# Optimization experiments

Measured on AMD Instinct MI355X. Metric: run time of the kernel, lower is better.

The kernel has to match this reference:

```python
import jax, jax.numpy as jnp
import numpy as np

N_NODES = 100000


def _add_self_loops(edge_index, n):
    loop = jnp.arange(n, dtype=edge_index.dtype)
    src = jnp.concatenate([edge_index[0], loop])
    dst = jnp.concatenate([edge_index[1], loop])
    return src, dst


def _gcn_conv(x, src, dst, n, W, b):
    # PyG GCNConv: linear first, then sym-normalized aggregation, then bias.
    h = x @ W                                   # [N, out]
    deg = jnp.zeros((n,), h.dtype).at[dst].add(1.0)   # in-degree incl. self-loops
    dinv = jnp.where(deg > 0, jax.lax.rsqrt(deg), 0.0)
    norm = dinv[src] * dinv[dst]                # [E+N]
    msg = h[src] * norm[:, None]                # gather + scale
    out = jax.ops.segment_sum(msg, dst, num_segments=n)  # scatter-add
    return out + b


def setup_inputs() -> dict:
    key = jax.random.key(0)
    ks = jax.random.split(key, 9)
    n, d_in, d_h, d_out = N_NODES, 64, 64, 64
    x = jax.random.normal(ks[0], (n, d_in), jnp.float32)
    edge_index = jax.random.randint(ks[1], (2, 1200000), 0, n, jnp.int64)
    s = lambda k, sh: jax.random.normal(k, sh, jnp.float32) * (1.0 / np.sqrt(sh[0]))
    return {
        "x": x,
        "edge_index": edge_index,
        "W1": s(ks[2], (d_in, d_h)),
        "b1": jnp.zeros((d_h,), jnp.float32),
        "W2": s(ks[3], (d_h, d_out)),
        "b2": jnp.zeros((d_out,), jnp.float32),
        "Wl": s(ks[4], (d_out, d_out)),
        "bl": jnp.zeros((d_out,), jnp.float32),
    }


def reference(x, edge_index, W1, b1, W2, b2, Wl, bl):
    n = x.shape[0]
    src, dst = _add_self_loops(edge_index, n)
    h = _gcn_conv(x, src, dst, n, W1, b1)
    h = jax.nn.relu(h)
    h = _gcn_conv(h, src, dst, n, W2, b2)
    return h @ Wl + bl
```

## Files before the change

kernel.cpp:

```cpp
#include <hip/hip_runtime.h>
#include <hip/hip_bf16.h>


#define FEAT 64

typedef __attribute__((ext_vector_type(8))) short bf16x8;
typedef __attribute__((ext_vector_type(4))) float f32x4;
union BF8 { bf16x8 v; unsigned short u[8]; unsigned pk[4]; uint4 q; };

__device__ __forceinline__ unsigned short f2bf(float f) {
    unsigned u = __float_as_uint(f);
    return (unsigned short)((u + 0x7FFFu + ((u >> 16) & 1u)) >> 16);
}
__device__ __forceinline__ float bflo(unsigned u) { return __uint_as_float(u << 16); }
__device__ __forceinline__ float bfhi(unsigned u) { return __uint_as_float(u & 0xFFFF0000u); }
__device__ __forceinline__ unsigned pk2bf(float a, float b) {
    union { __hip_bfloat162 b; unsigned u; } cv;
    cv.b = __float22bfloat162_rn(make_float2(a, b));
    return cv.u;
}

__global__ void k_prepw(const float* __restrict__ W1, const float* __restrict__ W2,
                        const float* __restrict__ Wl, unsigned short* __restrict__ P,
                        int* __restrict__ bcnt) {
    if (blockIdx.x == 3) {
        if (threadIdx.x < 256) bcnt[threadIdx.x] = 0;
        return;
    }
    const float* W = (blockIdx.x == 0) ? W1 : (blockIdx.x == 1) ? W2 : Wl;
    unsigned short* p = P + blockIdx.x * 4096;
    for (int i = threadIdx.x; i < 4096; i += 256) {
        int c = i >> 10, s = (i >> 9) & 1, l = (i >> 3) & 63, j = i & 7;
        int k = s * 32 + ((l >> 4) << 3) + j;
        int col = ((l & 15) << 2) + c;
        p[i] = f2bf(W[k * 64 + col]);
    }
}

__global__ void __launch_bounds__(256)
k_bhist(const int* __restrict__ dst, int* __restrict__ bcnt, int E) {
    __shared__ int h[256];
    int tid = threadIdx.x;
    h[tid] = 0;
    __syncthreads();
    int stride = gridDim.x * 256;
    for (int e = blockIdx.x * 256 + tid; e < E; e += stride)
        atomicAdd(&h[dst[e] >> 9], 1);
    __syncthreads();
    if (h[tid]) atomicAdd(&bcnt[tid], h[tid]);
}

__global__ void k_bscan(const int* __restrict__ bcnt, int* __restrict__ bbase,
                        int* __restrict__ bcur) {
    __shared__ int s[256];
    int t = threadIdx.x;
    int v = bcnt[t];
    s[t] = v;
    __syncthreads();
    for (int off = 1; off < 256; off <<= 1) {
        int x = (t >= off) ? s[t - off] : 0;
        __syncthreads();
        s[t] += x;
        __syncthreads();
    }
    int ex = s[t] - v;
    bbase[t] = ex;
    bcur[t] = ex;
    if (t == 255) bbase[256] = s[255];
}

__global__ void __launch_bounds__(256)
k_part(const int* __restrict__ src, const int* __restrict__ dst,
       int* __restrict__ bcur, unsigned* __restrict__ pass1, int E) {
    __shared__ unsigned pk[4096];
    __shared__ unsigned char bk[4096];
    __shared__ int h[256];
    __shared__ int cur[256];
    int tid = threadIdx.x;
    h[tid] = 0;
    __syncthreads();
    int base = blockIdx.x * 4096;
#pragma unroll
    for (int i = 0; i < 16; ++i) {
        int li = i * 256 + tid;
        int e = base + li;
        if (e < E) {
            int s = src[e], d = dst[e];
            int b = d >> 9;
            pk[li] = ((unsigned)s << 9) | ((unsigned)d & 511u);
            bk[li] = (unsigned char)b;
            atomicAdd(&h[b], 1);
        } else {
            bk[li] = 255;
            pk[li] = 0xFFFFFFFFu;
        }
    }
    __syncthreads();
    {
        int c = h[tid];
        int run = c ? atomicAdd(&bcur[tid], c) : 0;
        cur[tid] = run;
    }
    __syncthreads();
#pragma unroll
    for (int i = 0; i < 16; ++i) {
        int li = i * 256 + tid;
        int e = base + li;
        if (e < E) {
            int b = bk[li];
            int pos = atomicAdd(&cur[b], 1);
            pass1[pos] = pk[li];
        }
    }
}

__global__ void __launch_bounds__(512)
k_csr(const unsigned* __restrict__ pass1, const int* __restrict__ bbase,
      int* __restrict__ offs, float* __restrict__ dinv, int* __restrict__ esrc,
      int n, int E) {
    __shared__ int hist[512];
    __shared__ int cur[512];
    int tid = threadIdx.x;
    int b = blockIdx.x;
    hist[tid] = 0;
    __syncthreads();
    int beg = bbase[b], end = bbase[b + 1];
    for (int j = beg + tid; j < end; j += 512)
        atomicAdd(&hist[pass1[j] & 511u], 1);
    __syncthreads();
    int v = hist[tid];
    for (int off = 1; off < 512; off <<= 1) {
        int x = (tid >= off) ? hist[tid - off] : 0;
        __syncthreads();
        hist[tid] += x;
        __syncthreads();
    }
    int excl = hist[tid] - v;
    int node = (b << 9) + tid;
    if (node < n) {
        offs[node] = beg + excl;
        dinv[node] = rsqrtf((float)v + 1.0f);
    }
    cur[tid] = excl;
    if (b == 0 && tid == 0) offs[n] = E;
    __syncthreads();
    for (int j = beg + tid; j < end; j += 512) {
        unsigned u = pass1[j];
        int loc = (int)(u & 511u);
        int r = atomicAdd(&cur[loc], 1);
        esrc[beg + r] = (int)(u >> 9);
    }
}

template <bool IN_BF16, bool OUT_F32, bool SCALE>
__global__ void __launch_bounds__(256)
k_gemm_mfma(const void* __restrict__ Xv, const unsigned short* __restrict__ Wpk,
            const float* __restrict__ bias, const float* __restrict__ rowscale,
            void* __restrict__ Hv, int n) {
    int lane = threadIdx.x & 63;
    int wid = (blockIdx.x << 2) + (threadIdx.x >> 6);
    int nw = gridDim.x << 2;
    int T = (n + 15) >> 4;
    BF8 bfr[8];
    const uint4* wp = (const uint4*)Wpk;
#pragma unroll
    for (int f = 0; f < 8; ++f) bfr[f].q = wp[f * 64 + lane];
    int mrow = lane & 15, kq = lane >> 4, colb = lane & 15;
    float4 bv4 = make_float4(0.f, 0.f, 0.f, 0.f);
    if (OUT_F32) bv4 = ((const float4*)bias)[colb];
    for (int t = wid; t < T; t += nw) {
        int rb = t << 4;
        int row = rb + mrow;
        bool ok = row < n;
        BF8 a0, a1;
        if (IN_BF16) {
            const uint4* xr = (const uint4*)((const unsigned short*)Xv + ((unsigned)row << 6));
            a0.q = ok ? xr[kq]     : make_uint4(0, 0, 0, 0);
            a1.q = ok ? xr[kq + 4] : make_uint4(0, 0, 0, 0);
        } else {
            const float4* xr = (const float4*)((const float*)Xv + ((unsigned)row << 6));
            float4 z = make_float4(0.f, 0.f, 0.f, 0.f);
            float4 p0 = ok ? xr[kq * 2]     : z;
            float4 p1 = ok ? xr[kq * 2 + 1] : z;
            float4 p2 = ok ? xr[8 + kq * 2] : z;
            float4 p3 = ok ? xr[8 + kq * 2 + 1] : z;
            a0.pk[0] = pk2bf(p0.x, p0.y); a0.pk[1] = pk2bf(p0.z, p0.w);
            a0.pk[2] = pk2bf(p1.x, p1.y); a0.pk[3] = pk2bf(p1.z, p1.w);
            a1.pk[0] = pk2bf(p2.x, p2.y); a1.pk[1] = pk2bf(p2.z, p2.w);
            a1.pk[2] = pk2bf(p3.x, p3.y); a1.pk[3] = pk2bf(p3.z, p3.w);
        }
        f32x4 acc0 = {0.f, 0.f, 0.f, 0.f}, acc1 = acc0, acc2 = acc0, acc3 = acc0;
        acc0 = __builtin_amdgcn_mfma_f32_16x16x32_bf16(a0.v, bfr[0].v, acc0, 0, 0, 0);
        acc0 = __builtin_amdgcn_mfma_f32_16x16x32_bf16(a1.v, bfr[1].v, acc0, 0, 0, 0);
        acc1 = __builtin_amdgcn_mfma_f32_16x16x32_bf16(a0.v, bfr[2].v, acc1, 0, 0, 0);
        acc1 = __builtin_amdgcn_mfma_f32_16x16x32_bf16(a1.v, bfr[3].v, acc1, 0, 0, 0);
        acc2 = __builtin_amdgcn_mfma_f32_16x16x32_bf16(a0.v, bfr[4].v, acc2, 0, 0, 0);
        acc2 = __builtin_amdgcn_mfma_f32_16x16x32_bf16(a1.v, bfr[5].v, acc2, 0, 0, 0);
        acc3 = __builtin_amdgcn_mfma_f32_16x16x32_bf16(a0.v, bfr[6].v, acc3, 0, 0, 0);
        acc3 = __builtin_amdgcn_mfma_f32_16x16x32_bf16(a1.v, bfr[7].v, acc3, 0, 0, 0);
        int rowb = rb + (kq << 2);
        if (OUT_F32) {
            float* O = (float*)Hv;
#pragma unroll
            for (int i = 0; i < 4; ++i) {
                if (rowb + i >= n) break;
                unsigned ro = (unsigned)(rowb + i) << 6;
                float4 o = make_float4(acc0[i] + bv4.x, acc1[i] + bv4.y,
                                       acc2[i] + bv4.z, acc3[i] + bv4.w);
                *(float4*)(O + ro + (colb << 2)) = o;
            }
        } else {
            unsigned short* O = (unsigned short*)Hv;
#pragma unroll
            for (int i = 0; i < 4; ++i) {
                if (rowb + i >= n) break;
                float sc = SCALE ? rowscale[rowb + i] : 1.0f;
                unsigned ro = (unsigned)(rowb + i) << 6;
                uint2 o = make_uint2(pk2bf(acc0[i] * sc, acc1[i] * sc),
                                     pk2bf(acc2[i] * sc, acc3[i] * sc));
                *(uint2*)(O + ro + (colb << 2)) = o;
            }
        }
    }
}

template <bool RELU>
__global__ void __launch_bounds__(256)
k_agg(const int* __restrict__ offs, const int* __restrict__ esrc,
      const float* __restrict__ dinv, const unsigned short* __restrict__ Hs,
      const float* __restrict__ bias, unsigned short* __restrict__ out, int n) {
    int lane = threadIdx.x & 63;
    int h8 = lane & 7;
    int node = blockIdx.x * 32 + ((threadIdx.x >> 6) << 3) + (lane >> 3);
    bool nok = node < n;
    int beg = 0, end = 0;
    if (nok) { beg = offs[node]; end = offs[node + 1]; }
    float a0 = 0.f, a1 = 0.f, a2 = 0.f, a3 = 0.f, a4 = 0.f, a5 = 0.f, a6 = 0.f, a7 = 0.f;
    int j = beg;
    int s0 = 0, s1 = 0, s2 = 0, s3 = 0;
    float w0 = 0.f, w1 = 0.f, w2 = 0.f, w3 = 0.f;
    if (j     < end) { s0 = esrc[j];     w0 = 1.f; }
    if (j + 1 < end) { s1 = esrc[j + 1]; w1 = 1.f; }
    if (j + 2 < end) { s2 = esrc[j + 2]; w2 = 1.f; }
    if (j + 3 < end) { s3 = esrc[j + 3]; w3 = 1.f; }
    while (__ballot(j < end)) {
        uint4 h0 = *(const uint4*)(Hs + ((unsigned)s0 << 6) + (h8 << 3));
        uint4 h1 = *(const uint4*)(Hs + ((unsigned)s1 << 6) + (h8 << 3));
        uint4 h2 = *(const uint4*)(Hs + ((unsigned)s2 << 6) + (h8 << 3));
        uint4 h3 = *(const uint4*)(Hs + ((unsigned)s3 << 6) + (h8 << 3));
        int jn = j + 4;
        int t0 = s0, t1 = s1, t2 = s2, t3 = s3;
        float v0 = 0.f, v1 = 0.f, v2 = 0.f, v3 = 0.f;
        if (jn     < end) { t0 = esrc[jn];     v0 = 1.f; }
        if (jn + 1 < end) { t1 = esrc[jn + 1]; v1 = 1.f; }
        if (jn + 2 < end) { t2 = esrc[jn + 2]; v2 = 1.f; }
        if (jn + 3 < end) { t3 = esrc[jn + 3]; v3 = 1.f; }
        a0 = fmaf(bflo(h0.x), w0, a0); a1 = fmaf(bfhi(h0.x), w0, a1);
        a2 = fmaf(bflo(h0.y), w0, a2); a3 = fmaf(bfhi(h0.y), w0, a3);
        a4 = fmaf(bflo(h0.z), w0, a4); a5 = fmaf(bfhi(h0.z), w0, a5);
        a6 = fmaf(bflo(h0.w), w0, a6); a7 = fmaf(bfhi(h0.w), w0, a7);
        a0 = fmaf(bflo(h1.x), w1, a0); a1 = fmaf(bfhi(h1.x), w1, a1);
        a2 = fmaf(bflo(h1.y), w1, a2); a3 = fmaf(bfhi(h1.y), w1, a3);
        a4 = fmaf(bflo(h1.z), w1, a4); a5 = fmaf(bfhi(h1.z), w1, a5);
        a6 = fmaf(bflo(h1.w), w1, a6); a7 = fmaf(bfhi(h1.w), w1, a7);
        a0 = fmaf(bflo(h2.x), w2, a0); a1 = fmaf(bfhi(h2.x), w2, a1);
        a2 = fmaf(bflo(h2.y), w2, a2); a3 = fmaf(bfhi(h2.y), w2, a3);
        a4 = fmaf(bflo(h2.z), w2, a4); a5 = fmaf(bfhi(h2.z), w2, a5);
        a6 = fmaf(bflo(h2.w), w2, a6); a7 = fmaf(bfhi(h2.w), w2, a7);
        a0 = fmaf(bflo(h3.x), w3, a0); a1 = fmaf(bfhi(h3.x), w3, a1);
        a2 = fmaf(bflo(h3.y), w3, a2); a3 = fmaf(bfhi(h3.y), w3, a3);
        a4 = fmaf(bflo(h3.z), w3, a4); a5 = fmaf(bfhi(h3.z), w3, a5);
        a6 = fmaf(bflo(h3.w), w3, a6); a7 = fmaf(bfhi(h3.w), w3, a7);
        j = jn;
        s0 = t0; s1 = t1; s2 = t2; s3 = t3;
        w0 = v0; w1 = v1; w2 = v2; w3 = v3;
    }
    if (nok) {
        float dd = dinv[node];
        uint4 sv = *(const uint4*)(Hs + ((unsigned)node << 6) + (h8 << 3));
        const float4* b4 = (const float4*)bias;
        float4 bA = b4[h8 * 2], bB = b4[h8 * 2 + 1];
        float r0 = (a0 + bflo(sv.x)) * dd + bA.x;
        float r1 = (a1 + bfhi(sv.x)) * dd + bA.y;
        float r2 = (a2 + bflo(sv.y)) * dd + bA.z;
        float r3 = (a3 + bfhi(sv.y)) * dd + bA.w;
        float r4 = (a4 + bflo(sv.z)) * dd + bB.x;
        float r5 = (a5 + bfhi(sv.z)) * dd + bB.y;
        float r6 = (a6 + bflo(sv.w)) * dd + bB.z;
        float r7 = (a7 + bfhi(sv.w)) * dd + bB.w;
        if (RELU) {
            r0 = fmaxf(r0, 0.f); r1 = fmaxf(r1, 0.f); r2 = fmaxf(r2, 0.f); r3 = fmaxf(r3, 0.f);
            r4 = fmaxf(r4, 0.f); r5 = fmaxf(r5, 0.f); r6 = fmaxf(r6, 0.f); r7 = fmaxf(r7, 0.f);
        }
        uint4 o = make_uint4(pk2bf(r0, r1), pk2bf(r2, r3), pk2bf(r4, r5), pk2bf(r6, r7));
        *(uint4*)(out + ((unsigned)node << 6) + (h8 << 3)) = o;
    }
}

extern "C" void kernel_launch(void* const* d_in, const int* in_sizes, int n_in,
                              void* d_out, int out_size, void* d_ws, size_t ws_size,
                              hipStream_t stream) {
    const float* x  = (const float*)d_in[0];
    const int*   ei = (const int*)d_in[1];
    const float* W1 = (const float*)d_in[2];
    const float* b1 = (const float*)d_in[3];
    const float* W2 = (const float*)d_in[4];
    const float* b2 = (const float*)d_in[5];
    const float* Wl = (const float*)d_in[6];
    const float* bl = (const float*)d_in[7];
    float* out = (float*)d_out;

    const int n = in_sizes[0] / FEAT;
    const int E = in_sizes[1] / 2;
    const int* src = ei;
    const int* dst = ei + E;

    const int B = 256;
    const int NB = (n + 511) >> 9;
    const int pblocks = (E + 4095) / 4096;
    const int agg_blocks  = (n + 31) / 32;
    const int T = (n + 15) / 16;
    const int gemm_blocks = (T + 7) / 8;

    char* w = (char*)d_ws;
    int*   bcnt     = (int*)w;              w += 256 * 4;
    int*   bbase    = (int*)w;              w += 260 * 4;
    int*   bcur     = (int*)w;              w += 256 * 4;
    int*   offs     = (int*)w;              w += ((size_t)n + 4) * 4;
    float* dinv     = (float*)w;            w += (size_t)n * 4;
    w = (char*)(((uintptr_t)w + 15) & ~(uintptr_t)15);
    unsigned short* Wpk = (unsigned short*)w;  w += 3 * 4096 * 2;
    unsigned* pass1 = (unsigned*)w;         w += (size_t)E * 4;
    int*   esrc     = (int*)w;              w += (size_t)E * 4;
    unsigned short* bufA = (unsigned short*)w;  w += (size_t)n * FEAT * 2;
    unsigned short* bufB = (unsigned short*)w;

    k_prepw<<<dim3(4), dim3(B), 0, stream>>>(W1, W2, Wl, Wpk, bcnt);

    k_bhist<<<dim3(256), dim3(B), 0, stream>>>(dst, bcnt, E);
    k_bscan<<<dim3(1), dim3(B), 0, stream>>>(bcnt, bbase, bcur);
    k_part<<<dim3(pblocks), dim3(B), 0, stream>>>(src, dst, bcur, pass1, E);
    k_csr<<<dim3(NB), dim3(512), 0, stream>>>(pass1, bbase, offs, dinv, esrc, n, E);

    k_gemm_mfma<false, false, true><<<dim3(gemm_blocks), dim3(B), 0, stream>>>(x, Wpk, nullptr, dinv, bufA, n);
    k_agg<true><<<dim3(agg_blocks), dim3(B), 0, stream>>>(offs, esrc, dinv, bufA, b1, bufB, n);

    k_gemm_mfma<true, false, true><<<dim3(gemm_blocks), dim3(B), 0, stream>>>(bufB, Wpk + 4096, nullptr, dinv, bufA, n);
    k_agg<false><<<dim3(agg_blocks), dim3(B), 0, stream>>>(offs, esrc, dinv, bufA, b2, bufB, n);

    k_gemm_mfma<true, true, false><<<dim3(gemm_blocks), dim3(B), 0, stream>>>(bufB, Wpk + 8192, bl, nullptr, out, n);
}
```

Before: 251.5 us.

## Fuse aggregation with following GEMM and degree-sort nodes for load balance

Aggregation kernels now apply the next layer's weight matrix via MFMA on an LDS tile, removing two standalone GEMM launches and the round trip of intermediate features through memory. Nodes within each 512-node bucket are reordered by in-degree (perm, pofs, pdinv) so that lanes in a wave share similar edge counts and spend less time idle. The weight prep is merged into the partition kernel as extra blocks, and the bucket histogram writes per-block partials instead of using global atomics, which drops the bcnt zeroing launch. The cost is indirect permuted writes, extra per-node metadata, and a block-wide sync inside the aggregation.

```diff
diff --git a/kernel.cpp b/kernel.cpp
--- a/kernel.cpp
+++ b/kernel.cpp
@@ -3,6 +3,7 @@
 
 
 #define FEAT 64
+#define NBH 128
 
 typedef __attribute__((ext_vector_type(8))) short bf16x8;
 typedef __attribute__((ext_vector_type(4))) float f32x4;
@@ -20,25 +21,8 @@
     return cv.u;
 }
 
-__global__ void k_prepw(const float* __restrict__ W1, const float* __restrict__ W2,
-                        const float* __restrict__ Wl, unsigned short* __restrict__ P,
-                        int* __restrict__ bcnt) {
-    if (blockIdx.x == 3) {
-        if (threadIdx.x < 256) bcnt[threadIdx.x] = 0;
-        return;
-    }
-    const float* W = (blockIdx.x == 0) ? W1 : (blockIdx.x == 1) ? W2 : Wl;
-    unsigned short* p = P + blockIdx.x * 4096;
-    for (int i = threadIdx.x; i < 4096; i += 256) {
-        int c = i >> 10, s = (i >> 9) & 1, l = (i >> 3) & 63, j = i & 7;
-        int k = s * 32 + ((l >> 4) << 3) + j;
-        int col = ((l & 15) << 2) + c;
-        p[i] = f2bf(W[k * 64 + col]);
-    }
-}
-
 __global__ void __launch_bounds__(256)
-k_bhist(const int* __restrict__ dst, int* __restrict__ bcnt, int E) {
+k_bhist(const int* __restrict__ dst, int* __restrict__ bh, int E) {
     __shared__ int h[256];
     int tid = threadIdx.x;
     h[tid] = 0;
@@ -47,14 +31,15 @@
     for (int e = blockIdx.x * 256 + tid; e < E; e += stride)
         atomicAdd(&h[dst[e] >> 9], 1);
     __syncthreads();
-    if (h[tid]) atomicAdd(&bcnt[tid], h[tid]);
-}
-
-__global__ void k_bscan(const int* __restrict__ bcnt, int* __restrict__ bbase,
+    bh[blockIdx.x * 256 + tid] = h[tid];
+}
+
+__global__ void k_bscan(const int* __restrict__ bh, int* __restrict__ bbase,
                         int* __restrict__ bcur) {
     __shared__ int s[256];
     int t = threadIdx.x;
-    int v = bcnt[t];
+    int v = 0;
+    for (int b = 0; b < NBH; ++b) v += bh[b * 256 + t];
     s[t] = v;
     __syncthreads();
     for (int off = 1; off < 256; off <<= 1) {
@@ -71,7 +56,21 @@
 
 __global__ void __launch_bounds__(256)
 k_part(const int* __restrict__ src, const int* __restrict__ dst,
-       int* __restrict__ bcur, unsigned* __restrict__ pass1, int E) {
+       int* __restrict__ bcur, unsigned* __restrict__ pass1, int E, int pblocks,
+       const float* __restrict__ W1, const float* __restrict__ W2,
+       const float* __restrict__ Wl, unsigned short* __restrict__ P) {
+    if ((int)blockIdx.x >= pblocks) {
+        int widx = blockIdx.x - pblocks;
+        const float* W = (widx == 0) ? W1 : (widx == 1) ? W2 : Wl;
+        unsigned short* p = P + widx * 4096;
+        for (int i = threadIdx.x; i < 4096; i += 256) {
+            int c = i >> 10, s = (i >> 9) & 1, l = (i >> 3) & 63, j = i & 7;
+            int k = s * 32 + ((l >> 4) << 3) + j;
+            int col = ((l & 15) << 2) + c;
+            p[i] = f2bf(W[k * 64 + col]);
+        }
+        return;
+    }
     __shared__ unsigned pk[4096];
     __shared__ unsigned char bk[4096];
     __shared__ int h[256];
@@ -116,13 +115,18 @@
 
 __global__ void __launch_bounds__(512)
 k_csr(const unsigned* __restrict__ pass1, const int* __restrict__ bbase,
-      int* __restrict__ offs, float* __restrict__ dinv, int* __restrict__ esrc,
+      float* __restrict__ dinv, int* __restrict__ esrc,
+      int* __restrict__ perm, int2* __restrict__ pofs, float* __restrict__ pdinv,
       int n, int E) {
     __shared__ int hist[512];
     __shared__ int cur[512];
+    __shared__ int dh[64];
+    __shared__ int dbase[64];
+    __shared__ int dcur[64];
     int tid = threadIdx.x;
     int b = blockIdx.x;
     hist[tid] = 0;
+    if (tid < 64) dh[tid] = 0;
     __syncthreads();
     int beg = bbase[b], end = bbase[b + 1];
     for (int j = beg + tid; j < end; j += 512)
@@ -137,13 +141,26 @@
     }
     int excl = hist[tid] - v;
     int node = (b << 9) + tid;
-    if (node < n) {
-        offs[node] = beg + excl;
+    bool valid = node < n;
+    if (valid) {
         dinv[node] = rsqrtf((float)v + 1.0f);
+        atomicAdd(&dh[min(v, 63)], 1);
     }
     cur[tid] = excl;
-    if (b == 0 && tid == 0) offs[n] = E;
-    __syncthreads();
+    __syncthreads();
+    if (tid == 0) {
+        int run = 0;
+        for (int i = 0; i < 64; ++i) { dbase[i] = run; run += dh[i]; dcur[i] = 0; }
+    }
+    __syncthreads();
+    if (valid) {
+        int bin = min(v, 63);
+        int r = atomicAdd(&dcur[bin], 1);
+        int gs = (b << 9) + dbase[bin] + r;
+        perm[gs] = node;
+        pofs[gs] = make_int2(beg + excl, beg + excl + v);
+        pdinv[gs] = rsqrtf((float)v + 1.0f);
+    }
     for (int j = beg + tid; j < end; j += 512) {
         unsigned u = pass1[j];
         int loc = (int)(u & 511u);
@@ -224,61 +241,84 @@
     }
 }
 
-template <bool RELU>
+template <bool RELU, bool OUT_F32>
 __global__ void __launch_bounds__(256)
-k_agg(const int* __restrict__ offs, const int* __restrict__ esrc,
-      const float* __restrict__ dinv, const unsigned short* __restrict__ Hs,
-      const float* __restrict__ bias, unsigned short* __restrict__ out, int n) {
-    int lane = threadIdx.x & 63;
+k_fagg(const int* __restrict__ perm, const int2* __restrict__ pofs,
+       const float* __restrict__ pdinv, const int* __restrict__ esrc,
+       const unsigned short* __restrict__ Hs, const float* __restrict__ bias1,
+       const unsigned short* __restrict__ Wpk, const float* __restrict__ bias2,
+       void* __restrict__ outv, int n) {
+    __shared__ uint4 lds_a[32][8];
+    int tid = threadIdx.x;
+    int lane = tid & 63;
+    int wv = tid >> 6;
     int h8 = lane & 7;
-    int node = blockIdx.x * 32 + ((threadIdx.x >> 6) << 3) + (lane >> 3);
-    bool nok = node < n;
-    int beg = 0, end = 0;
-    if (nok) { beg = offs[node]; end = offs[node + 1]; }
+    int rl = (wv << 3) + (lane >> 3);
+    int slot = blockIdx.x * 32 + rl;
+    bool ok = slot < n;
+    int node = 0, beg = 0, end = 0;
+    float dd = 0.f;
+    if (ok) {
+        node = perm[slot];
+        int2 oe = pofs[slot];
+        beg = oe.x; end = oe.y;
+        dd = pdinv[slot];
+    }
+    int hh = wv & 1, tt = wv >> 1;
+    BF8 bq0, bq1, bq2, bq3;
+    {
+        const uint4* wp = (const uint4*)Wpk;
+        bq0.q = wp[(4 * hh + 0) * 64 + lane];
+        bq1.q = wp[(4 * hh + 1) * 64 + lane];
+        bq2.q = wp[(4 * hh + 2) * 64 + lane];
+        bq3.q = wp[(4 * hh + 3) * 64 + lane];
+    }
     float a0 = 0.f, a1 = 0.f, a2 = 0.f, a3 = 0.f, a4 = 0.f, a5 = 0.f, a6 = 0.f, a7 = 0.f;
-    int j = beg;
-    int s0 = 0, s1 = 0, s2 = 0, s3 = 0;
-    float w0 = 0.f, w1 = 0.f, w2 = 0.f, w3 = 0.f;
-    if (j     < end) { s0 = esrc[j];     w0 = 1.f; }
-    if (j + 1 < end) { s1 = esrc[j + 1]; w1 = 1.f; }
-    if (j + 2 < end) { s2 = esrc[j + 2]; w2 = 1.f; }
-    if (j + 3 < end) { s3 = esrc[j + 3]; w3 = 1.f; }
-    while (__ballot(j < end)) {
-        uint4 h0 = *(const uint4*)(Hs + ((unsigned)s0 << 6) + (h8 << 3));
-        uint4 h1 = *(const uint4*)(Hs + ((unsigned)s1 << 6) + (h8 << 3));
-        uint4 h2 = *(const uint4*)(Hs + ((unsigned)s2 << 6) + (h8 << 3));
-        uint4 h3 = *(const uint4*)(Hs + ((unsigned)s3 << 6) + (h8 << 3));
-        int jn = j + 4;
-        int t0 = s0, t1 = s1, t2 = s2, t3 = s3;
-        float v0 = 0.f, v1 = 0.f, v2 = 0.f, v3 = 0.f;
-        if (jn     < end) { t0 = esrc[jn];     v0 = 1.f; }
-        if (jn + 1 < end) { t1 = esrc[jn + 1]; v1 = 1.f; }
-        if (jn + 2 < end) { t2 = esrc[jn + 2]; v2 = 1.f; }
-        if (jn + 3 < end) { t3 = esrc[jn + 3]; v3 = 1.f; }
-        a0 = fmaf(bflo(h0.x), w0, a0); a1 = fmaf(bfhi(h0.x), w0, a1);
-        a2 = fmaf(bflo(h0.y), w0, a2); a3 = fmaf(bfhi(h0.y), w0, a3);
-        a4 = fmaf(bflo(h0.z), w0, a4); a5 = fmaf(bfhi(h0.z), w0, a5);
-        a6 = fmaf(bflo(h0.w), w0, a6); a7 = fmaf(bfhi(h0.w), w0, a7);
-        a0 = fmaf(bflo(h1.x), w1, a0); a1 = fmaf(bfhi(h1.x), w1, a1);
-        a2 = fmaf(bflo(h1.y), w1, a2); a3 = fmaf(bfhi(h1.y), w1, a3);
-        a4 = fmaf(bflo(h1.z), w1, a4); a5 = fmaf(bfhi(h1.z), w1, a5);
-        a6 = fmaf(bflo(h1.w), w1, a6); a7 = fmaf(bfhi(h1.w), w1, a7);
-        a0 = fmaf(bflo(h2.x), w2, a0); a1 = fmaf(bfhi(h2.x), w2, a1);
-        a2 = fmaf(bflo(h2.y), w2, a2); a3 = fmaf(bfhi(h2.y), w2, a3);
-        a4 = fmaf(bflo(h2.z), w2, a4); a5 = fmaf(bfhi(h2.z), w2, a5);
-        a6 = fmaf(bflo(h2.w), w2, a6); a7 = fmaf(bfhi(h2.w), w2, a7);
-        a0 = fmaf(bflo(h3.x), w3, a0); a1 = fmaf(bfhi(h3.x), w3, a1);
-        a2 = fmaf(bflo(h3.y), w3, a2); a3 = fmaf(bfhi(h3.y), w3, a3);
-        a4 = fmaf(bflo(h3.z), w3, a4); a5 = fmaf(bfhi(h3.z), w3, a5);
-        a6 = fmaf(bflo(h3.w), w3, a6); a7 = fmaf(bfhi(h3.w), w3, a7);
-        j = jn;
-        s0 = t0; s1 = t1; s2 = t2; s3 = t3;
-        w0 = v0; w1 = v1; w2 = v2; w3 = v3;
-    }
-    if (nok) {
-        float dd = dinv[node];
+    {
+        int j = beg;
+        int s0 = 0, s1 = 0, s2 = 0, s3 = 0;
+        float w0 = 0.f, w1 = 0.f, w2 = 0.f, w3 = 0.f;
+        if (j     < end) { s0 = esrc[j];     w0 = 1.f; }
+        if (j + 1 < end) { s1 = esrc[j + 1]; w1 = 1.f; }
+        if (j + 2 < end) { s2 = esrc[j + 2]; w2 = 1.f; }
+        if (j + 3 < end) { s3 = esrc[j + 3]; w3 = 1.f; }
+        while (__ballot(j < end)) {
+            uint4 h0 = *(const uint4*)(Hs + ((unsigned)s0 << 6) + (h8 << 3));
+            uint4 h1 = *(const uint4*)(Hs + ((unsigned)s1 << 6) + (h8 << 3));
+            uint4 h2 = *(const uint4*)(Hs + ((unsigned)s2 << 6) + (h8 << 3));
+            uint4 h3 = *(const uint4*)(Hs + ((unsigned)s3 << 6) + (h8 << 3));
+            int jn = j + 4;
+            int t0 = s0, t1 = s1, t2 = s2, t3 = s3;
+            float v0 = 0.f, v1 = 0.f, v2 = 0.f, v3 = 0.f;
+            if (jn     < end) { t0 = esrc[jn];     v0 = 1.f; }
+            if (jn + 1 < end) { t1 = esrc[jn + 1]; v1 = 1.f; }
+            if (jn + 2 < end) { t2 = esrc[jn + 2]; v2 = 1.f; }
+            if (jn + 3 < end) { t3 = esrc[jn + 3]; v3 = 1.f; }
+            a0 = fmaf(bflo(h0.x), w0, a0); a1 = fmaf(bfhi(h0.x), w0, a1);
+            a2 = fmaf(bflo(h0.y), w0, a2); a3 = fmaf(bfhi(h0.y), w0, a3);
+            a4 = fmaf(bflo(h0.z), w0, a4); a5 = fmaf(bfhi(h0.z), w0, a5);
+            a6 = fmaf(bflo(h0.w), w0, a6); a7 = fmaf(bfhi(h0.w), w0, a7);
+            a0 = fmaf(bflo(h1.x), w1, a0); a1 = fmaf(bfhi(h1.x), w1, a1);
+            a2 = fmaf(bflo(h1.y), w1, a2); a3 = fmaf(bfhi(h1.y), w1, a3);
+            a4 = fmaf(bflo(h1.z), w1, a4); a5 = fmaf(bfhi(h1.z), w1, a5);
+            a6 = fmaf(bflo(h1.w), w1, a6); a7 = fmaf(bfhi(h1.w), w1, a7);
+            a0 = fmaf(bflo(h2.x), w2, a0); a1 = fmaf(bfhi(h2.x), w2, a1);
+            a2 = fmaf(bflo(h2.y), w2, a2); a3 = fmaf(bfhi(h2.y), w2, a3);
+            a4 = fmaf(bflo(h2.z), w2, a4); a5 = fmaf(bfhi(h2.z), w2, a5);
+            a6 = fmaf(bflo(h2.w), w2, a6); a7 = fmaf(bfhi(h2.w), w2, a7);
+            a0 = fmaf(bflo(h3.x), w3, a0); a1 = fmaf(bfhi(h3.x), w3, a1);
+            a2 = fmaf(bflo(h3.y), w3, a2); a3 = fmaf(bfhi(h3.y), w3, a3);
+            a4 = fmaf(bflo(h3.z), w3, a4); a5 = fmaf(bfhi(h3.z), w3, a5);
+            a6 = fmaf(bflo(h3.w), w3, a6); a7 = fmaf(bfhi(h3.w), w3, a7);
+            j = jn;
+            s0 = t0; s1 = t1; s2 = t2; s3 = t3;
+            w0 = v0; w1 = v1; w2 = v2; w3 = v3;
+        }
+    }
+    uint4 packed = make_uint4(0, 0, 0, 0);
+    if (ok) {
         uint4 sv = *(const uint4*)(Hs + ((unsigned)node << 6) + (h8 << 3));
-        const float4* b4 = (const float4*)bias;
+        const float4* b4 = (const float4*)bias1;
         float4 bA = b4[h8 * 2], bB = b4[h8 * 2 + 1];
         float r0 = (a0 + bflo(sv.x)) * dd + bA.x;
         float r1 = (a1 + bfhi(sv.x)) * dd + bA.y;
@@ -292,8 +332,39 @@
             r0 = fmaxf(r0, 0.f); r1 = fmaxf(r1, 0.f); r2 = fmaxf(r2, 0.f); r3 = fmaxf(r3, 0.f);
             r4 = fmaxf(r4, 0.f); r5 = fmaxf(r5, 0.f); r6 = fmaxf(r6, 0.f); r7 = fmaxf(r7, 0.f);
         }
-        uint4 o = make_uint4(pk2bf(r0, r1), pk2bf(r2, r3), pk2bf(r4, r5), pk2bf(r6, r7));
-        *(uint4*)(out + ((unsigned)node << 6) + (h8 << 3)) = o;
+        packed = make_uint4(pk2bf(r0, r1), pk2bf(r2, r3), pk2bf(r4, r5), pk2bf(r6, r7));
+    }
+    lds_a[rl][h8 ^ (rl & 7)] = packed;
+    __syncthreads();
+    int mr = lane & 15, kq = lane >> 4, colb = lane & 15;
+    int rloc = tt * 16 + mr;
+    BF8 fa0, fa1;
+    fa0.q = lds_a[rloc][kq ^ (rloc & 7)];
+    fa1.q = lds_a[rloc][(kq + 4) ^ (rloc & 7)];
+    f32x4 accA = {0.f, 0.f, 0.f, 0.f}, accB = accA;
+    accA = __builtin_amdgcn_mfma_f32_16x16x32_bf16(fa0.v, bq0.v, accA, 0, 0, 0);
+    accA = __builtin_amdgcn_mfma_f32_16x16x32_bf16(fa1.v, bq1.v, accA, 0, 0, 0);
+    accB = __builtin_amdgcn_mfma_f32_16x16x32_bf16(fa0.v, bq2.v, accB, 0, 0, 0);
+    accB = __builtin_amdgcn_mfma_f32_16x16x32_bf16(fa1.v, bq3.v, accB, 0, 0, 0);
+    float b2x = 0.f, b2y = 0.f;
+    if (OUT_F32) {
+        b2x = bias2[(colb << 2) + (hh << 1)];
+        b2y = bias2[(colb << 2) + (hh << 1) + 1];
+    }
+    int rowb = tt * 16 + (kq << 2);
+#pragma unroll
+    for (int i = 0; i < 4; ++i) {
+        int sl = blockIdx.x * 32 + rowb + i;
+        if (sl >= n) break;
+        int orow = perm[sl];
+        if (OUT_F32) {
+            float2 o = make_float2(accA[i] + b2x, accB[i] + b2y);
+            *(float2*)((float*)outv + ((unsigned)orow << 6) + (colb << 2) + (hh << 1)) = o;
+        } else {
+            float sc = pdinv[sl];
+            unsigned o = pk2bf(accA[i] * sc, accB[i] * sc);
+            *(unsigned*)((unsigned short*)outv + ((unsigned)orow << 6) + (colb << 2) + (hh << 1)) = o;
+        }
     }
 }
 
@@ -318,35 +389,39 @@
     const int B = 256;
     const int NB = (n + 511) >> 9;
     const int pblocks = (E + 4095) / 4096;
-    const int agg_blocks  = (n + 31) / 32;
+    const int fagg_blocks = (n + 31) / 32;
     const int T = (n + 15) / 16;
     const int gemm_blocks = (T + 7) / 8;
 
     char* w = (char*)d_ws;
-    int*   bcnt     = (int*)w;              w += 256 * 4;
+    int*   bh       = (int*)w;              w += NBH * 256 * 4;
     int*   bbase    = (int*)w;              w += 260 * 4;
     int*   bcur     = (int*)w;              w += 256 * 4;
-    int*   offs     = (int*)w;              w += ((size_t)n + 4) * 4;
     float* dinv     = (float*)w;            w += (size_t)n * 4;
+    float* pdinv    = (float*)w;            w += (size_t)n * 4;
+    int*   perm     = (int*)w;              w += (size_t)n * 4;
     w = (char*)(((uintptr_t)w + 15) & ~(uintptr_t)15);
+    int2*  pofs     = (int2*)w;             w += (size_t)n * 8;
     unsigned short* Wpk = (unsigned short*)w;  w += 3 * 4096 * 2;
+    w = (char*)(((uintptr_t)w + 15) & ~(uintptr_t)15);
     unsigned* pass1 = (unsigned*)w;         w += (size_t)E * 4;
     int*   esrc     = (int*)w;              w += (size_t)E * 4;
     unsigned short* bufA = (unsigned short*)w;  w += (size_t)n * FEAT * 2;
     unsigned short* bufB = (unsigned short*)w;
 
-    k_prepw<<<dim3(4), dim3(B), 0, stream>>>(W1, W2, Wl, Wpk, bcnt);
-
-    k_bhist<<<dim3(256), dim3(B), 0, stream>>>(dst, bcnt, E);
-    k_bscan<<<dim3(1), dim3(B), 0, stream>>>(bcnt, bbase, bcur);
-    k_part<<<dim3(pblocks), dim3(B), 0, stream>>>(src, dst, bcur, pass1, E);
-    k_csr<<<dim3(NB), dim3(512), 0, stream>>>(pass1, bbase, offs, dinv, esrc, n, E);
-
-    k_gemm_mfma<false, false, true><<<dim3(gemm_blocks), dim3(B), 0, stream>>>(x, Wpk, nullptr, dinv, bufA, n);
-    k_agg<true><<<dim3(agg_blocks), dim3(B), 0, stream>>>(offs, esrc, dinv, bufA, b1, bufB, n);
-
-    k_gemm_mfma<true, false, true><<<dim3(gemm_blocks), dim3(B), 0, stream>>>(bufB, Wpk + 4096, nullptr, dinv, bufA, n);
-    k_agg<false><<<dim3(agg_blocks), dim3(B), 0, stream>>>(offs, esrc, dinv, bufA, b2, bufB, n);
-
-    k_gemm_mfma<true, true, false><<<dim3(gemm_blocks), dim3(B), 0, stream>>>(bufB, Wpk + 8192, bl, nullptr, out, n);
-}
+    k_bhist<<<dim3(NBH), dim3(B), 0, stream>>>(dst, bh, E);
+    k_bscan<<<dim3(1), dim3(B), 0, stream>>>(bh, bbase, bcur);
+    k_part<<<dim3(pblocks + 3), dim3(B), 0, stream>>>(src, dst, bcur, pass1, E,
+                                                      pblocks, W1, W2, Wl, Wpk);
+    k_csr<<<dim3(NB), dim3(512), 0, stream>>>(pass1, bbase, dinv, esrc,
+                                              perm, pofs, pdinv, n, E);
+
+    k_gemm_mfma<false, false, true><<<dim3(gemm_blocks), dim3(B), 0, stream>>>(
+        x, Wpk, nullptr, dinv, bufA, n);
+
+    k_fagg<true, false><<<dim3(fagg_blocks), dim3(B), 0, stream>>>(
+        perm, pofs, pdinv, esrc, bufA, b1, Wpk + 4096, nullptr, bufB, n);
+
+    k_fagg<false, true><<<dim3(fagg_blocks), dim3(B), 0, stream>>>(
+        perm, pofs, pdinv, esrc, bufB, b2, Wpk + 8192, bl, out, n);
+}
```

Result: no change. 255.1 us (+1.5%).
